# Optimization experiments

Hardware: AMD Instinct MI355X
Metric: run time of the kernel (lower is better)

## Reference

```python
import jax, jax.numpy as jnp
import numpy as np

N_NODES = 100000
N_EDGES = 1600000
IN_F = 128
OUT_F = 64
K = 2


def _propagate(x, src, dst, num_nodes):
    """GCN propagation with self-loops already appended to (src, dst).
    out[j] = sum_{(i->j)} deg(i)^-1/2 * deg(j)^-1/2 * x[i]
    where deg is the in-degree counting self-loops (PyG gcn_norm)."""
    deg = jnp.zeros((num_nodes,), dtype=x.dtype).at[dst].add(1.0)
    dinv = jnp.where(deg > 0, jax.lax.rsqrt(deg), 0.0)
    norm = dinv[src] * dinv[dst]                      # [E+N]
    msg = x[src] * norm[:, None]                      # gather + scale
    return jnp.zeros_like(x).at[dst].add(msg)         # scatter-add


def setup_inputs() -> dict:
    key = jax.random.key(0)
    k1, k2, k3, k4 = jax.random.split(key, 4)
    x = jax.random.normal(k1, (N_NODES, IN_F), dtype=jnp.float32)
    edge_index = jax.random.randint(k2, (2, N_EDGES), 0, N_NODES, dtype=jnp.int64)
    # Linear weights, torch convention: y = x @ W.T, W is [out, in]
    W1 = jax.random.normal(k3, (IN_F, IN_F), dtype=jnp.float32) / np.sqrt(IN_F)
    W2 = jax.random.normal(k4, (OUT_F, IN_F), dtype=jnp.float32) / np.sqrt(IN_F)
    return {"x": x, "edge_index": edge_index, "W1": W1, "W2": W2}


def reference(x, edge_index, W1, W2):
    num_nodes = x.shape[0]
    # add self loops once (same augmented edge set used by P1 and P2)
    loop = jnp.arange(num_nodes, dtype=edge_index.dtype)
    src = jnp.concatenate([edge_index[0], loop])
    dst = jnp.concatenate([edge_index[1], loop])
    for _ in range(K):
        x = x @ W1.T
        x = _propagate(x, src, dst, num_nodes)
    x = x @ W2.T
    x = _propagate(x, src, dst, num_nodes)
    # original computes log_softmax into `out` but returns pre-softmax x
    return x
```

## Files before the change

### kernel.cpp

```cpp
#include <hip/hip_runtime.h>

#define NN 100000
#define NE 1600000
#define ENT (NE + NN)
#define NB 196
#define BINCAP 10240


__global__ void probe_kernel(const unsigned* __restrict__ edges, int* __restrict__ flag) {
    if (threadIdx.x == 0 && blockIdx.x == 0) {
        int is64 = 1;
        for (int i = 1; i < 64; i += 2)
            if (edges[i] != 0u) { is64 = 0; break; }
        *flag = is64;
    }
}


__global__ __launch_bounds__(256) void part_kernel(const void* __restrict__ edges,
                                                   const int* __restrict__ flag,
                                                   int2* __restrict__ binned,
                                                   int* __restrict__ binCnt) {
    __shared__ int hist[NB], base[NB], rank[NB];
    int t = threadIdx.x;
    for (int i = t; i < NB; i += 256) hist[i] = 0;
    __syncthreads();
    int i0 = blockIdx.x * 4096;
    bool is64 = (*flag != 0);
    int s[16], d[16];
    #pragma unroll
    for (int q = 0; q < 16; ++q) {
        int i = i0 + q * 256 + t;
        if (i < NE) {
            if (is64) {
                s[q] = (int)((const long long*)edges)[i];
                d[q] = (int)((const long long*)edges)[NE + i];
            } else {
                s[q] = ((const int*)edges)[i];
                d[q] = ((const int*)edges)[NE + i];
            }
            atomicAdd(&hist[d[q] >> 9], 1);
        } else d[q] = -1;
    }
    __syncthreads();
    for (int i = t; i < NB; i += 256) {
        base[i] = atomicAdd(&binCnt[i], hist[i]);
        rank[i] = 0;
    }
    __syncthreads();
    #pragma unroll
    for (int q = 0; q < 16; ++q) {
        if (d[q] >= 0) {
            int b = d[q] >> 9;
            int r = base[b] + atomicAdd(&rank[b], 1);
            if (r < BINCAP) binned[(size_t)b * BINCAP + r] = make_int2(s[q], d[q]);
        }
    }
}


__global__ void binscan_kernel(const int* __restrict__ binCnt, int* __restrict__ binOff) {
    __shared__ int sh[256];
    int t = threadIdx.x;
    int nodes = (t < NB) ? ((t == NB - 1) ? (NN - 512 * (NB - 1)) : 512) : 0;
    int v = (t < NB) ? binCnt[t] + nodes : 0;
    sh[t] = v;
    __syncthreads();
    for (int off = 1; off < 256; off <<= 1) {
        int a = (t >= off) ? sh[t - off] : 0;
        __syncthreads();
        sh[t] += a;
        __syncthreads();
    }
    if (t < NB) binOff[t] = sh[t] - v;
    if (t == NB - 1) binOff[NB] = sh[t];
}


__global__ __launch_bounds__(1024) void degscan_kernel(const int2* __restrict__ binned,
                                                       const int* __restrict__ binCnt,
                                                       const int* __restrict__ binOff,
                                                       float* __restrict__ dinv,
                                                       int* __restrict__ rowoff) {
    __shared__ int hist[512];
    __shared__ int sc[512];
    int b = blockIdx.x, t = threadIdx.x;
    int nb0 = b << 9;
    int nNodes = min(512, NN - nb0);
    int cnt = binCnt[b];
    if (t < 512) hist[t] = 0;
    __syncthreads();
    const int2* e = binned + (size_t)b * BINCAP;
    for (int i = t; i < cnt; i += 1024) atomicAdd(&hist[e[i].y - nb0], 1);
    __syncthreads();
    int v = 0;
    if (t < 512) { v = (t < nNodes) ? hist[t] + 1 : 0; sc[t] = v; }
    __syncthreads();
    for (int off = 1; off < 512; off <<= 1) {
        int a = (t >= off && t < 512) ? sc[t - off] : 0;
        __syncthreads();
        if (t < 512) sc[t] += a;
        __syncthreads();
    }
    if (t < nNodes) {
        dinv[nb0 + t] = rsqrtf((float)(hist[t] + 1));
        rowoff[nb0 + t] = binOff[b] + sc[t] - v;
    }
    if (b == NB - 1 && t == 0) rowoff[NN] = ENT;
}


__global__ __launch_bounds__(1024) void fill2_kernel(const int2* __restrict__ binned,
                                                     const int* __restrict__ binCnt,
                                                     const int* __restrict__ binOff,
                                                     const float* __restrict__ dinv,
                                                     const int* __restrict__ rowoff,
                                                     int2* __restrict__ edge) {
    extern __shared__ char smem[];
    int2* stage = (int2*)smem;
    int*  cur   = (int*)(smem + (size_t)BINCAP * 8);
    int b = blockIdx.x, t = threadIdx.x;
    int nb0 = b << 9;
    int nNodes = min(512, NN - nb0);
    int cnt = binCnt[b];
    int off0 = binOff[b];
    int total = binOff[b + 1] - off0;
    if (t < nNodes) {
        int lo = rowoff[nb0 + t] - off0;
        float di = dinv[nb0 + t];
        stage[lo] = make_int2(nb0 + t, __float_as_int(di * di));
        cur[t] = lo + 1;
    }
    __syncthreads();
    const int2* e = binned + (size_t)b * BINCAP;
    for (int i = t; i < cnt; i += 1024) {
        int2 sd = e[i];
        int slot = atomicAdd(&cur[sd.y - nb0], 1);
        float v = dinv[sd.x] * dinv[sd.y];
        if (slot < BINCAP) stage[slot] = make_int2(sd.x, __float_as_int(v));
    }
    __syncthreads();
    int2* dst = edge + off0;
    for (int i = t; i < total; i += 1024) dst[i] = stage[i];
}


__global__ __launch_bounds__(256) void wprod1_kernel(const float* __restrict__ W1,
                                                     const float* __restrict__ W2,
                                                     float* __restrict__ T) {
    int idx = blockIdx.x * blockDim.x + threadIdx.x;
    if (idx >= 128 * 64) return;
    int k = idx >> 6, j = idx & 63;
    float s = 0.f;
    #pragma unroll 8
    for (int q = 0; q < 128; ++q)
        s += W1[q * 128 + k] * W2[j * 128 + q];
    T[k * 64 + j] = s;
}

__global__ __launch_bounds__(256) void wprod2_kernel(const float* __restrict__ W1,
                                                     const float* __restrict__ T,
                                                     float* __restrict__ WcT) {
    int idx = blockIdx.x * blockDim.x + threadIdx.x;
    if (idx >= 128 * 64) return;
    int i = idx >> 6, j = idx & 63;
    float s = 0.f;
    #pragma unroll 8
    for (int k = 0; k < 128; ++k)
        s += W1[k * 128 + i] * T[k * 64 + j];
    WcT[j * 128 + i] = s;
}


__global__ __launch_bounds__(256) void spmm64_kernel(const int* __restrict__ rowoff,
                                                     const int2* __restrict__ edge,
                                                     const float* __restrict__ H,
                                                     float* __restrict__ O) {
    int w = (int)((blockIdx.x * (unsigned)blockDim.x + threadIdx.x) >> 6);
    if (w >= NN) return;
    int lane = threadIdx.x & 63;
    int s = rowoff[w], e = rowoff[w + 1];
    float acc = 0.f;
    const float* base = H + lane;

    int p = s;
    for (; p + 8 <= e; p += 8) {
        int2 E[8];
        #pragma unroll
        for (int q = 0; q < 8; ++q) E[q] = edge[p + q];
        #pragma unroll
        for (int q = 0; q < 8; ++q)
            acc += __int_as_float(E[q].y) * base[(size_t)E[q].x * 64];
    }
    if (p + 4 <= e) {
        int2 E[4];
        #pragma unroll
        for (int q = 0; q < 4; ++q) E[q] = edge[p + q];
        #pragma unroll
        for (int q = 0; q < 4; ++q)
            acc += __int_as_float(E[q].y) * base[(size_t)E[q].x * 64];
        p += 4;
    }
    for (; p < e; ++p) {
        int2 E = edge[p];
        acc += __int_as_float(E.y) * base[(size_t)E.x * 64];
    }
    O[(size_t)w * 64 + lane] = acc;
}


template<int N>
__global__ __launch_bounds__(256) void gemm_xwt(const float* __restrict__ X,
                                                const float* __restrict__ W,
                                                float* __restrict__ Y, int M) {
    constexpr int K = 128, BM = 64, BK = 32;
    constexpr int TM = 4, TN = N / 16;
    __shared__ float Xs[BK][BM + 4];
    __shared__ float Ws[BK][N + 4];
    int t  = threadIdx.x;
    int m0 = blockIdx.x * BM;
    int r0 = (t >> 4) * TM;
    int c0 = (t & 15) * TN;
    float acc[TM][TN] = {};
    for (int k0 = 0; k0 < K; k0 += BK) {
        #pragma unroll
        for (int i = 0; i < 2; ++i) {
            int f  = t + i * 256;
            int m  = f >> 3;
            int kq = (f & 7) << 2;
            int gm = m0 + m; if (gm >= M) gm = M - 1;
            float4 v = *(const float4*)&X[(size_t)gm * K + k0 + kq];
            Xs[kq + 0][m] = v.x; Xs[kq + 1][m] = v.y;
            Xs[kq + 2][m] = v.z; Xs[kq + 3][m] = v.w;
        }
        #pragma unroll
        for (int i = 0; i < N / 32; ++i) {
            int f  = t + i * 256;
            int n  = f >> 3;
            int kq = (f & 7) << 2;
            float4 v = *(const float4*)&W[(size_t)n * K + k0 + kq];
            Ws[kq + 0][n] = v.x; Ws[kq + 1][n] = v.y;
            Ws[kq + 2][n] = v.z; Ws[kq + 3][n] = v.w;
        }
        __syncthreads();
        #pragma unroll
        for (int k = 0; k < BK; ++k) {
            float4 xv = *(const float4*)&Xs[k][r0];
            float xf[TM] = {xv.x, xv.y, xv.z, xv.w};
            float wf[TN];
            #pragma unroll
            for (int j = 0; j < TN; j += 4) {
                float4 wv = *(const float4*)&Ws[k][c0 + j];
                wf[j] = wv.x; wf[j + 1] = wv.y; wf[j + 2] = wv.z; wf[j + 3] = wv.w;
            }
            #pragma unroll
            for (int i = 0; i < TM; ++i)
                #pragma unroll
                for (int j = 0; j < TN; ++j)
                    acc[i][j] += xf[i] * wf[j];
        }
        __syncthreads();
    }
    #pragma unroll
    for (int i = 0; i < TM; ++i) {
        int gm = m0 + r0 + i;
        if (gm < M) {
            #pragma unroll
            for (int j = 0; j < TN; j += 4) {
                float4 v = {acc[i][j], acc[i][j + 1], acc[i][j + 2], acc[i][j + 3]};
                *(float4*)&Y[(size_t)gm * N + c0 + j] = v;
            }
        }
    }
}


extern "C" void kernel_launch(void* const* d_in, const int* in_sizes, int n_in,
                              void* d_out, int out_size, void* d_ws, size_t ws_size,
                              hipStream_t stream) {
    const float* x     = (const float*)d_in[0];
    const void*  edges = d_in[1];
    const float* W1    = (const float*)d_in[2];
    const float* W2    = (const float*)d_in[3];
    float* out = (float*)d_out;

    char* ws = (char*)d_ws;
    size_t off = 0;
    auto take = [&](size_t bytes) -> char* {
        char* p = ws + off;
        off = (off + bytes + 255) & ~(size_t)255;
        return p;
    };
    int*   flag   = (int*)take(4);
    int*   binCnt = (int*)take((size_t)NB * 4);
    int*   binOff = (int*)take((size_t)(NB + 1) * 4);
    float* dinv   = (float*)take((size_t)NN * 4);
    int*   rowoff = (int*)take((size_t)(NN + 1) * 4);
    float* Tbuf   = (float*)take((size_t)128 * 64 * 4);
    float* WcT    = (float*)take((size_t)64 * 128 * 4);
    int2*  binned = (int2*)take((size_t)NB * BINCAP * 8);
    int2*  edgeA  = (int2*)take((size_t)ENT * 8);
    float* h      = (float*)take((size_t)NN * 64 * 4);
    float* y      = (float*)take((size_t)NN * 64 * 4);
    if (off > ws_size) return;

    hipMemsetAsync(binCnt, 0, (size_t)NB * 4, stream);
    probe_kernel<<<1, 64, 0, stream>>>((const unsigned*)edges, flag);
    wprod1_kernel<<<32, 256, 0, stream>>>(W1, W2, Tbuf);
    wprod2_kernel<<<32, 256, 0, stream>>>(W1, Tbuf, WcT);
    part_kernel<<<(NE + 4095) / 4096, 256, 0, stream>>>(edges, flag, binned, binCnt);
    binscan_kernel<<<1, 256, 0, stream>>>(binCnt, binOff);
    degscan_kernel<<<NB, 1024, 0, stream>>>(binned, binCnt, binOff, dinv, rowoff);
    size_t f2lds = (size_t)BINCAP * 8 + 512 * 4;
    fill2_kernel<<<NB, 1024, f2lds, stream>>>(binned, binCnt, binOff, dinv, rowoff, edgeA);

    const int GB = (NN + 63) / 64;
    const int PB = (NN * 64 + 255) / 256;

    gemm_xwt<64><<<GB, 256, 0, stream>>>(x, WcT, h, NN);
    spmm64_kernel<<<PB, 256, 0, stream>>>(rowoff, edgeA, h, y);
    spmm64_kernel<<<PB, 256, 0, stream>>>(rowoff, edgeA, y, h);
    spmm64_kernel<<<PB, 256, 0, stream>>>(rowoff, edgeA, h, out);
}
```

Measured before the change: 287.8 us.

## Factor GCN normalization into row scaling and pack CSR to column-only indices

```diff
diff --git a/kernel.cpp b/kernel.cpp
--- a/kernel.cpp
+++ b/kernel.cpp
@@ -7,8 +7,11 @@
 #define BINCAP 10240
 
 
-__global__ void probe_kernel(const unsigned* __restrict__ edges, int* __restrict__ flag) {
-    if (threadIdx.x == 0 && blockIdx.x == 0) {
+__global__ void probe_zero(const unsigned* __restrict__ edges, int* __restrict__ flag,
+                           int* __restrict__ binCnt) {
+    int t = threadIdx.x;
+    if (t < NB) binCnt[t] = 0;
+    if (t == 0) {
         int is64 = 1;
         for (int i = 1; i < 64; i += 2)
             if (edges[i] != 0u) { is64 = 0; break; }
@@ -19,7 +22,7 @@
 
 __global__ __launch_bounds__(256) void part_kernel(const void* __restrict__ edges,
                                                    const int* __restrict__ flag,
-                                                   int2* __restrict__ binned,
+                                                   int* __restrict__ binned,
                                                    int* __restrict__ binCnt) {
     __shared__ int hist[NB], base[NB], rank[NB];
     int t = threadIdx.x;
@@ -33,11 +36,11 @@
         int i = i0 + q * 256 + t;
         if (i < NE) {
             if (is64) {
-                s[q] = (int)((const long long*)edges)[i];
-                d[q] = (int)((const long long*)edges)[NE + i];
+                s[q] = (int)__builtin_nontemporal_load(&((const long long*)edges)[i]);
+                d[q] = (int)__builtin_nontemporal_load(&((const long long*)edges)[NE + i]);
             } else {
-                s[q] = ((const int*)edges)[i];
-                d[q] = ((const int*)edges)[NE + i];
+                s[q] = __builtin_nontemporal_load(&((const int*)edges)[i]);
+                d[q] = __builtin_nontemporal_load(&((const int*)edges)[NE + i]);
             }
             atomicAdd(&hist[d[q] >> 9], 1);
         } else d[q] = -1;
@@ -53,94 +56,73 @@
         if (d[q] >= 0) {
             int b = d[q] >> 9;
             int r = base[b] + atomicAdd(&rank[b], 1);
-            if (r < BINCAP) binned[(size_t)b * BINCAP + r] = make_int2(s[q], d[q]);
-        }
-    }
-}
-
-
-__global__ void binscan_kernel(const int* __restrict__ binCnt, int* __restrict__ binOff) {
-    __shared__ int sh[256];
-    int t = threadIdx.x;
-    int nodes = (t < NB) ? ((t == NB - 1) ? (NN - 512 * (NB - 1)) : 512) : 0;
-    int v = (t < NB) ? binCnt[t] + nodes : 0;
-    sh[t] = v;
-    __syncthreads();
-    for (int off = 1; off < 256; off <<= 1) {
-        int a = (t >= off) ? sh[t - off] : 0;
-        __syncthreads();
-        sh[t] += a;
-        __syncthreads();
-    }
-    if (t < NB) binOff[t] = sh[t] - v;
-    if (t == NB - 1) binOff[NB] = sh[t];
-}
-
-
-__global__ __launch_bounds__(1024) void degscan_kernel(const int2* __restrict__ binned,
-                                                       const int* __restrict__ binCnt,
-                                                       const int* __restrict__ binOff,
-                                                       float* __restrict__ dinv,
-                                                       int* __restrict__ rowoff) {
-    __shared__ int hist[512];
-    __shared__ int sc[512];
+            if (r < BINCAP)
+                binned[(size_t)b * BINCAP + r] = ((d[q] & 511) << 17) | s[q];
+        }
+    }
+}
+
+
+__global__ __launch_bounds__(1024) void build2_kernel(const int* __restrict__ binCnt,
+                                                      const int* __restrict__ binned,
+                                                      float* __restrict__ dinv,
+                                                      int* __restrict__ rowoff,
+                                                      int* __restrict__ edge) {
+    extern __shared__ char smem[];
+    int* stage = (int*)smem;
+    int* hist  = (int*)(smem + (size_t)BINCAP * 4);
+    int* sc    = hist + 512;
+    int* cur   = sc + 512;
+    int* bsc   = cur + 512;
     int b = blockIdx.x, t = threadIdx.x;
     int nb0 = b << 9;
     int nNodes = min(512, NN - nb0);
-    int cnt = binCnt[b];
+
+    if (t < 256) {
+        int nodes = (t < NB) ? min(512, NN - (t << 9)) : 0;
+        bsc[t] = (t < NB) ? binCnt[t] + nodes : 0;
+    }
     if (t < 512) hist[t] = 0;
     __syncthreads();
-    const int2* e = binned + (size_t)b * BINCAP;
-    for (int i = t; i < cnt; i += 1024) atomicAdd(&hist[e[i].y - nb0], 1);
+    for (int off = 1; off < 256; off <<= 1) {
+        int a = (t < 256 && t >= off) ? bsc[t - off] : 0;
+        __syncthreads();
+        if (t < 256) bsc[t] += a;
+        __syncthreads();
+    }
+    int cntRaw = binCnt[b];
+    int cnt = min(cntRaw, BINCAP);
+    int off0 = bsc[b] - (cntRaw + nNodes);
+
+    const int* e = binned + (size_t)b * BINCAP;
+    for (int i = t; i < cnt; i += 1024) atomicAdd(&hist[e[i] >> 17], 1);
     __syncthreads();
     int v = 0;
     if (t < 512) { v = (t < nNodes) ? hist[t] + 1 : 0; sc[t] = v; }
     __syncthreads();
     for (int off = 1; off < 512; off <<= 1) {
-        int a = (t >= off && t < 512) ? sc[t - off] : 0;
+        int a = (t < 512 && t >= off) ? sc[t - off] : 0;
         __syncthreads();
         if (t < 512) sc[t] += a;
         __syncthreads();
     }
     if (t < nNodes) {
         dinv[nb0 + t] = rsqrtf((float)(hist[t] + 1));
-        rowoff[nb0 + t] = binOff[b] + sc[t] - v;
+        int lo = sc[t] - v;
+        rowoff[nb0 + t] = off0 + lo;
+        stage[lo] = nb0 + t;
+        cur[t] = lo + 1;
     }
     if (b == NB - 1 && t == 0) rowoff[NN] = ENT;
-}
-
-
-__global__ __launch_bounds__(1024) void fill2_kernel(const int2* __restrict__ binned,
-                                                     const int* __restrict__ binCnt,
-                                                     const int* __restrict__ binOff,
-                                                     const float* __restrict__ dinv,
-                                                     const int* __restrict__ rowoff,
-                                                     int2* __restrict__ edge) {
-    extern __shared__ char smem[];
-    int2* stage = (int2*)smem;
-    int*  cur   = (int*)(smem + (size_t)BINCAP * 8);
-    int b = blockIdx.x, t = threadIdx.x;
-    int nb0 = b << 9;
-    int nNodes = min(512, NN - nb0);
-    int cnt = binCnt[b];
-    int off0 = binOff[b];
-    int total = binOff[b + 1] - off0;
-    if (t < nNodes) {
-        int lo = rowoff[nb0 + t] - off0;
-        float di = dinv[nb0 + t];
-        stage[lo] = make_int2(nb0 + t, __float_as_int(di * di));
-        cur[t] = lo + 1;
-    }
-    __syncthreads();
-    const int2* e = binned + (size_t)b * BINCAP;
+    __syncthreads();
     for (int i = t; i < cnt; i += 1024) {
-        int2 sd = e[i];
-        int slot = atomicAdd(&cur[sd.y - nb0], 1);
-        float v = dinv[sd.x] * dinv[sd.y];
-        if (slot < BINCAP) stage[slot] = make_int2(sd.x, __float_as_int(v));
-    }
-    __syncthreads();
-    int2* dst = edge + off0;
+        int pk = e[i];
+        int slot = atomicAdd(&cur[pk >> 17], 1);
+        if (slot < BINCAP) stage[slot] = pk & 0x1FFFF;
+    }
+    __syncthreads();
+    int total = min(cntRaw + nNodes, BINCAP);
+    int* dst = edge + off0;
     for (int i = t; i < total; i += 1024) dst[i] = stage[i];
 }
 
@@ -172,48 +154,49 @@
 }
 
 
-__global__ __launch_bounds__(256) void spmm64_kernel(const int* __restrict__ rowoff,
-                                                     const int2* __restrict__ edge,
-                                                     const float* __restrict__ H,
-                                                     float* __restrict__ O) {
+template<int SPOW>
+__global__ __launch_bounds__(256) void spmm64f_kernel(const int* __restrict__ rowoff,
+                                                      const int* __restrict__ col,
+                                                      const float* __restrict__ dinv,
+                                                      const float* __restrict__ H,
+                                                      float* __restrict__ O) {
     int w = (int)((blockIdx.x * (unsigned)blockDim.x + threadIdx.x) >> 6);
     if (w >= NN) return;
     int lane = threadIdx.x & 63;
-    int s = rowoff[w], e = rowoff[w + 1];
+    int s = __builtin_amdgcn_readfirstlane(rowoff[w]);
+    int e = __builtin_amdgcn_readfirstlane(rowoff[w + 1]);
     float acc = 0.f;
     const float* base = H + lane;
 
     int p = s;
     for (; p + 8 <= e; p += 8) {
-        int2 E[8];
-        #pragma unroll
-        for (int q = 0; q < 8; ++q) E[q] = edge[p + q];
-        #pragma unroll
-        for (int q = 0; q < 8; ++q)
-            acc += __int_as_float(E[q].y) * base[(size_t)E[q].x * 64];
+        int c[8];
+        #pragma unroll
+        for (int q = 0; q < 8; ++q) c[q] = __builtin_nontemporal_load(&col[p + q]);
+        #pragma unroll
+        for (int q = 0; q < 8; ++q) acc += base[(size_t)c[q] * 64];
     }
     if (p + 4 <= e) {
-        int2 E[4];
-        #pragma unroll
-        for (int q = 0; q < 4; ++q) E[q] = edge[p + q];
-        #pragma unroll
-        for (int q = 0; q < 4; ++q)
-            acc += __int_as_float(E[q].y) * base[(size_t)E[q].x * 64];
+        int c[4];
+        #pragma unroll
+        for (int q = 0; q < 4; ++q) c[q] = __builtin_nontemporal_load(&col[p + q]);
+        #pragma unroll
+        for (int q = 0; q < 4; ++q) acc += base[(size_t)c[q] * 64];
         p += 4;
     }
-    for (; p < e; ++p) {
-        int2 E = edge[p];
-        acc += __int_as_float(E.y) * base[(size_t)E.x * 64];
-    }
-    O[(size_t)w * 64 + lane] = acc;
-}
-
-
-template<int N>
-__global__ __launch_bounds__(256) void gemm_xwt(const float* __restrict__ X,
-                                                const float* __restrict__ W,
-                                                float* __restrict__ Y, int M) {
-    constexpr int K = 128, BM = 64, BK = 32;
+    for (; p < e; ++p) acc += base[(size_t)__builtin_nontemporal_load(&col[p]) * 64];
+
+    float di = dinv[w];
+    float scale = (SPOW == 2) ? di * di : di;
+    __builtin_nontemporal_store(acc * scale, &O[(size_t)w * 64 + lane]);
+}
+
+
+__global__ __launch_bounds__(256) void gemm_xwt64_kernel(const float* __restrict__ X,
+                                                         const float* __restrict__ W,
+                                                         const float* __restrict__ dinv,
+                                                         float* __restrict__ Y, int M) {
+    constexpr int N = 64, K = 128, BM = 64, BK = 32;
     constexpr int TM = 4, TN = N / 16;
     __shared__ float Xs[BK][BM + 4];
     __shared__ float Ws[BK][N + 4];
@@ -265,9 +248,11 @@
     for (int i = 0; i < TM; ++i) {
         int gm = m0 + r0 + i;
         if (gm < M) {
+            float di = dinv[gm];
             #pragma unroll
             for (int j = 0; j < TN; j += 4) {
-                float4 v = {acc[i][j], acc[i][j + 1], acc[i][j + 2], acc[i][j + 3]};
+                float4 v = {di * acc[i][j], di * acc[i][j + 1],
+                            di * acc[i][j + 2], di * acc[i][j + 3]};
                 *(float4*)&Y[(size_t)gm * N + c0 + j] = v;
             }
         }
@@ -293,32 +278,28 @@
     };
     int*   flag   = (int*)take(4);
     int*   binCnt = (int*)take((size_t)NB * 4);
-    int*   binOff = (int*)take((size_t)(NB + 1) * 4);
     float* dinv   = (float*)take((size_t)NN * 4);
     int*   rowoff = (int*)take((size_t)(NN + 1) * 4);
     float* Tbuf   = (float*)take((size_t)128 * 64 * 4);
     float* WcT    = (float*)take((size_t)64 * 128 * 4);
-    int2*  binned = (int2*)take((size_t)NB * BINCAP * 8);
-    int2*  edgeA  = (int2*)take((size_t)ENT * 8);
-    float* h      = (float*)take((size_t)NN * 64 * 4);
+    int*   binned = (int*)take((size_t)NB * BINCAP * 4);
+    int*   edgeA  = (int*)take((size_t)ENT * 4);
+    float* g      = (float*)take((size_t)NN * 64 * 4);
     float* y      = (float*)take((size_t)NN * 64 * 4);
     if (off > ws_size) return;
 
-    hipMemsetAsync(binCnt, 0, (size_t)NB * 4, stream);
-    probe_kernel<<<1, 64, 0, stream>>>((const unsigned*)edges, flag);
+    probe_zero<<<1, 256, 0, stream>>>((const unsigned*)edges, flag, binCnt);
     wprod1_kernel<<<32, 256, 0, stream>>>(W1, W2, Tbuf);
     wprod2_kernel<<<32, 256, 0, stream>>>(W1, Tbuf, WcT);
     part_kernel<<<(NE + 4095) / 4096, 256, 0, stream>>>(edges, flag, binned, binCnt);
-    binscan_kernel<<<1, 256, 0, stream>>>(binCnt, binOff);
-    degscan_kernel<<<NB, 1024, 0, stream>>>(binned, binCnt, binOff, dinv, rowoff);
-    size_t f2lds = (size_t)BINCAP * 8 + 512 * 4;
-    fill2_kernel<<<NB, 1024, f2lds, stream>>>(binned, binCnt, binOff, dinv, rowoff, edgeA);
+    size_t b2lds = (size_t)BINCAP * 4 + (512 * 3 + 256) * 4;
+    build2_kernel<<<NB, 1024, b2lds, stream>>>(binCnt, binned, dinv, rowoff, edgeA);
 
     const int GB = (NN + 63) / 64;
     const int PB = (NN * 64 + 255) / 256;
 
-    gemm_xwt<64><<<GB, 256, 0, stream>>>(x, WcT, h, NN);
-    spmm64_kernel<<<PB, 256, 0, stream>>>(rowoff, edgeA, h, y);
-    spmm64_kernel<<<PB, 256, 0, stream>>>(rowoff, edgeA, y, h);
-    spmm64_kernel<<<PB, 256, 0, stream>>>(rowoff, edgeA, h, out);
-}
+    gemm_xwt64_kernel<<<GB, 256, 0, stream>>>(x, WcT, dinv, g, NN);
+    spmm64f_kernel<2><<<PB, 256, 0, stream>>>(rowoff, edgeA, dinv, g, y);
+    spmm64f_kernel<2><<<PB, 256, 0, stream>>>(rowoff, edgeA, dinv, y, g);
+    spmm64f_kernel<1><<<PB, 256, 0, stream>>>(rowoff, edgeA, dinv, g, out);
+}
```

Result: faster. 262.8 us (-8.7%).
